# Optimization experiments

Measured on AMD Instinct MI355X. Metric: run time of the kernel, lower is better.

The kernel has to match this reference:

```python
import jax, jax.numpy as jnp
import numpy as np

B, T, D, NH = 16, 1024, 2048, 4
H_CYCLES, L_CYCLES = 2, 2


def _ln(x, g, b, eps=1e-5):
    m = jnp.mean(x, axis=-1, keepdims=True)
    v = jnp.mean((x - m) ** 2, axis=-1, keepdims=True)
    return (x - m) * jax.lax.rsqrt(v + eps) * g + b


def _mha(q_in, k_in, v_in, in_w, in_b, out_w, out_b):
    # torch nn.MultiheadAttention (batch_first) with packed in_proj
    d = q_in.shape[-1]
    hd = d // NH
    wq, wk, wv = jnp.split(in_w, 3, axis=0)
    bq, bk, bv = jnp.split(in_b, 3, axis=0)
    q = (q_in @ wq.T + bq).reshape(q_in.shape[0], -1, NH, hd)
    k = (k_in @ wk.T + bk).reshape(k_in.shape[0], -1, NH, hd)
    v = (v_in @ wv.T + bv).reshape(v_in.shape[0], -1, NH, hd)
    att = jnp.einsum('bqhd,bkhd->bhqk', q, k) / jnp.sqrt(jnp.asarray(hd, q.dtype))
    att = jax.nn.softmax(att, axis=-1)
    o = jnp.einsum('bhqk,bkhd->bqhd', att, v).reshape(q_in.shape[0], -1, d)
    return o @ out_w.T + out_b


def _block(z, inj, p):
    # CoTReasoningBlock
    x = z + inj
    n1 = _ln(x, p['n1_g'], p['n1_b'])
    x = x + _mha(n1, n1, n1, p['attn_in_w'], p['attn_in_b'], p['attn_out_w'], p['attn_out_b'])
    n2 = _ln(x, p['n2_g'], p['n2_b'])
    h = jax.nn.gelu(n2 @ p['f1_w'].T + p['f1_b'], approximate=False)
    return x + h @ p['f2_w'].T + p['f2_b']


def setup_inputs() -> dict:
    key = jax.random.key(0)
    ks = iter(jax.random.split(key, 32))

    def w(*shape):
        return jax.random.normal(next(ks), shape, jnp.float32) * 0.02

    inp = {}
    inp['x'] = jax.random.normal(next(ks), (B, T, D), jnp.float32)
    inp['global_query'] = w(1, 1, D)
    inp['attn_in_w'] = w(3 * D, D)
    inp['attn_in_b'] = jnp.zeros((3 * D,), jnp.float32)
    inp['attn_out_w'] = w(D, D)
    inp['attn_out_b'] = jnp.zeros((D,), jnp.float32)
    inp['mlp1_w'] = w(D, D)
    inp['mlp1_b'] = jnp.zeros((D,), jnp.float32)
    inp['mlp2_w'] = w(D, D)
    inp['mlp2_b'] = jnp.zeros((D,), jnp.float32)
    for pfx in ('h', 'l'):
        inp[pfx + '_attn_in_w'] = w(3 * D, D)
        inp[pfx + '_attn_in_b'] = jnp.zeros((3 * D,), jnp.float32)
        inp[pfx + '_attn_out_w'] = w(D, D)
        inp[pfx + '_attn_out_b'] = jnp.zeros((D,), jnp.float32)
        inp[pfx + '_n1_g'] = jnp.ones((D,), jnp.float32)
        inp[pfx + '_n1_b'] = jnp.zeros((D,), jnp.float32)
        inp[pfx + '_n2_g'] = jnp.ones((D,), jnp.float32)
        inp[pfx + '_n2_b'] = jnp.zeros((D,), jnp.float32)
        inp[pfx + '_f1_w'] = w(D, D)
        inp[pfx + '_f1_b'] = jnp.zeros((D,), jnp.float32)
        inp[pfx + '_f2_w'] = w(D, D)
        inp[pfx + '_f2_b'] = jnp.zeros((D,), jnp.float32)
    inp['norm_g'] = jnp.ones((D,), jnp.float32)
    inp['norm_b'] = jnp.zeros((D,), jnp.float32)
    return inp


def reference(x, global_query, attn_in_w, attn_in_b, attn_out_w, attn_out_b,
              mlp1_w, mlp1_b, mlp2_w, mlp2_b,
              h_attn_in_w, h_attn_in_b, h_attn_out_w, h_attn_out_b,
              h_n1_g, h_n1_b, h_n2_g, h_n2_b, h_f1_w, h_f1_b, h_f2_w, h_f2_b,
              l_attn_in_w, l_attn_in_b, l_attn_out_w, l_attn_out_b,
              l_n1_g, l_n1_b, l_n2_g, l_n2_b, l_f1_w, l_f1_b, l_f2_w, l_f2_b,
              norm_g, norm_b):
    Bd, Td, Dd = x.shape
    q = jnp.broadcast_to(global_query, (Bd, 1, Dd))
    a = _mha(q, x, x, attn_in_w, attn_in_b, attn_out_w, attn_out_b)  # (B,1,D)
    a = jax.nn.gelu(a @ mlp1_w.T + mlp1_b, approximate=False) @ mlp2_w.T + mlp2_b

    Hp = dict(attn_in_w=h_attn_in_w, attn_in_b=h_attn_in_b, attn_out_w=h_attn_out_w,
              attn_out_b=h_attn_out_b, n1_g=h_n1_g, n1_b=h_n1_b, n2_g=h_n2_g, n2_b=h_n2_b,
              f1_w=h_f1_w, f1_b=h_f1_b, f2_w=h_f2_w, f2_b=h_f2_b)
    Lp = dict(attn_in_w=l_attn_in_w, attn_in_b=l_attn_in_b, attn_out_w=l_attn_out_w,
              attn_out_b=l_attn_out_b, n1_g=l_n1_g, n1_b=l_n1_b, n2_g=l_n2_g, n2_b=l_n2_b,
              f1_w=l_f1_w, f1_b=l_f1_b, f2_w=l_f2_w, f2_b=l_f2_b)

    z0 = jnp.zeros((1, 1, Dd), x.dtype)

    def step(carry, xt):
        zH, zL = carry
        xt = xt[None]  # (1,1,D)
        zHn, zLn = zH, zL
        # torch.no_grad refinement phase. NOTE: the original code shadows the
        # loop variable `_`, so BOTH conditions test the inner L-cycle index;
        # with H_CYCLES==L_CYCLES==2 the last L cycle is skipped and the inner
        # zH update never fires. Reproduced exactly.
        for _h in range(H_CYCLES):
            for _l in range(L_CYCLES):
                if not (_l == H_CYCLES - 1 and _l == L_CYCLES - 1):
                    zLn = _block(zLn, zHn + xt, Lp)
            if L_CYCLES - 1 != H_CYCLES - 1:
                zHn = _block(zHn, zLn, Hp)
        zHg = jax.lax.stop_gradient(zHn)
        zLg = jax.lax.stop_gradient(zLn)
        # grad-enabled final updates
        zLg = _block(zLg, zHg + xt, Lp)
        zHg = _block(zHg, zLg, Hp)
        return (zHg, zLg), None

    (zH, zL), _ = jax.lax.scan(step, (z0, z0), a)
    return _ln(zH, norm_g, norm_b)  # (1,1,D)
```

## Files before the change

### kernel.cpp

```cpp
#include <hip/hip_runtime.h>
#include <hip/hip_bf16.h>

#define DD 2048
#define SCALE 0.04419417382415922f


__device__ __forceinline__ float waveReduceSum(float v) {
  #pragma unroll
  for (int off = 32; off; off >>= 1) v += __shfl_down(v, off);
  return v;
}

__device__ __forceinline__ float blockReduceSum(float v, float* sred) {
  v = waveReduceSum(v);
  int wid = threadIdx.x >> 6, lane = threadIdx.x & 63;
  if (lane == 0) sred[wid] = v;
  __syncthreads();
  float r = (sred[0] + sred[1]) + (sred[2] + sred[3]);
  __syncthreads();
  return r;
}

__device__ __forceinline__ float geluf(float x) {
  return 0.5f * x * (1.0f + erff(x * 0.7071067811865476f));
}


__global__ void k_zero(float* p, int n) {
  int i = blockIdx.x * 256 + threadIdx.x;
  if (i < n) p[i] = 0.0f;
}


template<int NADD, bool LN, bool GELU, bool RES>
__launch_bounds__(256)
__global__ void gemv1(const float* __restrict__ W, const float* __restrict__ bias,
                      const float* __restrict__ v0, const float* __restrict__ v1,
                      const float* __restrict__ v2,
                      const float* __restrict__ g, const float* __restrict__ bln,
                      float* __restrict__ y, float* __restrict__ xside)
{
  __shared__ __align__(16) float sx[DD];
  __shared__ float sred[4];
  int tid = threadIdx.x;
  float xv[8];
  #pragma unroll
  for (int i = 0; i < 8; ++i) {
    int idx = tid + i * 256;
    float v = v0[idx];
    if (NADD >= 1) v += v1[idx];
    if (NADD >= 2) v += v2[idx];
    xv[i] = v;
  }
  if (xside != nullptr && blockIdx.x == 0) {
    #pragma unroll
    for (int i = 0; i < 8; ++i) xside[tid + i * 256] = xv[i];
  }
  if (LN) {
    float s = 0.0f;
    #pragma unroll
    for (int i = 0; i < 8; ++i) s += xv[i];
    float mean = blockReduceSum(s, sred) * (1.0f / DD);
    float vs = 0.0f;
    #pragma unroll
    for (int i = 0; i < 8; ++i) { float d = xv[i] - mean; vs += d * d; }
    float var = blockReduceSum(vs, sred) * (1.0f / DD);
    float rs = 1.0f / sqrtf(var + 1e-5f);
    #pragma unroll
    for (int i = 0; i < 8; ++i) {
      int idx = tid + i * 256;
      sx[idx] = (xv[i] - mean) * rs * g[idx] + bln[idx];
    }
  } else {
    #pragma unroll
    for (int i = 0; i < 8; ++i) sx[tid + i * 256] = xv[i];
  }
  __syncthreads();

  int wid = tid >> 6, lane = tid & 63;
  int row = blockIdx.x * 4 + wid;
  const float4* Wr = (const float4*)(W + (size_t)row * DD);
  const float4* sx4 = (const float4*)sx;
  float acc = 0.0f;
  #pragma unroll
  for (int i = 0; i < 8; ++i) {
    float4 w4 = Wr[lane + i * 64];
    float4 x4 = sx4[lane + i * 64];
    acc += w4.x * x4.x + w4.y * x4.y + w4.z * x4.z + w4.w * x4.w;
  }
  acc = waveReduceSum(acc);
  if (lane == 0) {
    float val = acc + bias[row];
    if (GELU) val = geluf(val);
    if (RES) y[row] += val; else y[row] = val;
  }
}


__global__ void k_ufold(const float* __restrict__ Wfull, const float* __restrict__ qv,
                        float* __restrict__ u)
{
  int seg = blockIdx.x & 15, chunk = blockIdx.x >> 4;
  int h = seg >> 2;
  int tid = threadIdx.x;
  __shared__ float sq[128];
  if (tid < 128) sq[tid] = qv[seg * 128 + tid];
  __syncthreads();
  int d = chunk * 256 + tid;
  const float* Wp = Wfull + (size_t)(2048 + seg * 128) * DD + d;
  float acc = 0.0f;
  #pragma unroll 4
  for (int j = 0; j < 128; ++j) acc += Wp[(size_t)j * DD] * sq[j];
  atomicAdd(&u[(h << 11) + d], acc * SCALE);
}

__global__ void k_cfold(const float* __restrict__ qv, const float* __restrict__ inb,
                        float* __restrict__ c)
{
  __shared__ float sred[4];
  int tid = threadIdx.x;
  for (int h = 0; h < 4; ++h) {
    float s = 0.0f;
    for (int j = tid; j < 512; j += 256) s += qv[h * 512 + j] * inb[2048 + h * 512 + j];
    float tot = blockReduceSum(s, sred);
    if (tid == 0) c[h] = tot * SCALE;
    __syncthreads();
  }
}


__global__ void k_scores(const float* __restrict__ x, const float* __restrict__ u,
                         const float* __restrict__ c, float* __restrict__ sc)
{
  int blk = blockIdx.x;
  int b = blk >> 10, t = blk & 1023;
  int tid = threadIdx.x, wid = tid >> 6, lane = tid & 63;
  const float4* xr = (const float4*)(x + (size_t)blk * DD);
  float acc[4] = {0, 0, 0, 0};
  #pragma unroll
  for (int i = 0; i < 2; ++i) {
    int f = tid + i * 256;
    float4 x4 = xr[f];
    #pragma unroll
    for (int h = 0; h < 4; ++h) {
      float4 u4 = ((const float4*)(u + (h << 11)))[f];
      acc[h] += x4.x * u4.x + x4.y * u4.y + x4.z * u4.z + x4.w * u4.w;
    }
  }
  __shared__ float sred[4][4];
  #pragma unroll
  for (int h = 0; h < 4; ++h) {
    float v = waveReduceSum(acc[h]);
    if (lane == 0) sred[h][wid] = v;
  }
  __syncthreads();
  if (tid < 4) {
    float v = sred[tid][0] + sred[tid][1] + sred[tid][2] + sred[tid][3] + c[tid];
    sc[((size_t)(b * 4 + tid) << 10) + t] = v;
  }
}


__global__ void k_softmax(float* __restrict__ s)
{
  __shared__ float sred[4];
  int tid = threadIdx.x, wid = tid >> 6, lane = tid & 63;
  float* p = s + ((size_t)blockIdx.x << 10);
  float v[4];
  #pragma unroll
  for (int i = 0; i < 4; ++i) v[i] = p[tid + i * 256];
  float m = fmaxf(fmaxf(v[0], v[1]), fmaxf(v[2], v[3]));
  #pragma unroll
  for (int off = 32; off; off >>= 1) m = fmaxf(m, __shfl_down(m, off));
  if (lane == 0) sred[wid] = m;
  __syncthreads();
  m = fmaxf(fmaxf(sred[0], sred[1]), fmaxf(sred[2], sred[3]));
  __syncthreads();
  float e[4], sum = 0.0f;
  #pragma unroll
  for (int i = 0; i < 4; ++i) { e[i] = expf(v[i] - m); sum += e[i]; }
  float tot = blockReduceSum(sum, sred);
  float inv = 1.0f / tot;
  #pragma unroll
  for (int i = 0; i < 4; ++i) p[tid + i * 256] = e[i] * inv;
}


__global__ void k_xbar_part(const float* __restrict__ x, const float* __restrict__ att,
                            float* __restrict__ part)
{
  int blk = blockIdx.x;
  int seg = blk & 7, chunk = (blk >> 3) & 7, b = blk >> 6;
  int tid = threadIdx.x;
  __shared__ float satt[4][128];
  for (int i = tid; i < 512; i += 256) {
    int h = i >> 7, j = i & 127;
    satt[h][j] = att[((size_t)(b * 4 + h) << 10) + seg * 128 + j];
  }
  __syncthreads();
  int d = chunk * 256 + tid;
  const float* xb = x + ((size_t)b * 1024 + seg * 128) * DD + d;
  float a0 = 0, a1 = 0, a2 = 0, a3 = 0;
  #pragma unroll 4
  for (int j = 0; j < 128; ++j) {
    float xv = xb[(size_t)j * DD];
    a0 += satt[0][j] * xv; a1 += satt[1][j] * xv;
    a2 += satt[2][j] * xv; a3 += satt[3][j] * xv;
  }
  size_t base = ((size_t)(b * 8 + seg) * 4);
  part[((base + 0) << 11) + d] = a0;
  part[((base + 1) << 11) + d] = a1;
  part[((base + 2) << 11) + d] = a2;
  part[((base + 3) << 11) + d] = a3;
}

__global__ void k_xbar_red(const float* __restrict__ part, float* __restrict__ xbar)
{
  int i = blockIdx.x * 256 + threadIdx.x;
  int d = i & 2047; int h = (i >> 11) & 3; int b = i >> 13;
  float s = 0.0f;
  #pragma unroll
  for (int seg = 0; seg < 8; ++seg)
    s += part[(((size_t)(b * 8 + seg) * 4 + h) << 11) + d];
  xbar[i] = s;
}


__launch_bounds__(256)
__global__ void k_vproj(const float* __restrict__ inW, const float* __restrict__ inB,
                        const float* __restrict__ xbar, float* __restrict__ o)
{
  __shared__ __align__(16) float sv[8][DD];
  int tid = threadIdx.x, wid = tid >> 6, lane = tid & 63;
  int row0 = blockIdx.x * 8;
  int h = row0 >> 9;
  int rowA = row0 + wid, rowB = row0 + 4 + wid;
  const float4* WA = (const float4*)(inW + (size_t)(4096 + rowA) * DD);
  const float4* WB = (const float4*)(inW + (size_t)(4096 + rowB) * DD);
  float4 wa[8], wb[8];
  #pragma unroll
  for (int i = 0; i < 8; ++i) { wa[i] = WA[lane + i * 64]; wb[i] = WB[lane + i * 64]; }
  float accA[16], accB[16];
  #pragma unroll
  for (int b = 0; b < 16; ++b) { accA[b] = 0; accB[b] = 0; }
  for (int half = 0; half < 2; ++half) {
    __syncthreads();
    for (int i = tid; i < 8 * 512; i += 256) {
      int b = i >> 9, f = i & 511;
      ((float4*)&sv[b][0])[f] =
          ((const float4*)(xbar + (((size_t)(half * 8 + b) * 4 + h) << 11)))[f];
    }
    __syncthreads();
    #pragma unroll
    for (int i = 0; i < 8; ++i) {
      int f = lane + i * 64;
      #pragma unroll
      for (int b = 0; b < 8; ++b) {
        float4 x4 = ((const float4*)&sv[b][0])[f];
        accA[half * 8 + b] += wa[i].x * x4.x + wa[i].y * x4.y + wa[i].z * x4.z + wa[i].w * x4.w;
        accB[half * 8 + b] += wb[i].x * x4.x + wb[i].y * x4.y + wb[i].z * x4.z + wb[i].w * x4.w;
      }
    }
  }
  #pragma unroll
  for (int b = 0; b < 16; ++b) {
    float v = waveReduceSum(accA[b]);
    if (lane == 0) o[((size_t)b << 11) + rowA] = v + inB[4096 + rowA];
    v = waveReduceSum(accB[b]);
    if (lane == 0) o[((size_t)b << 11) + rowB] = v + inB[4096 + rowB];
  }
}


template<bool GELU>
__launch_bounds__(256)
__global__ void gemvB(const float* __restrict__ W, const float* __restrict__ bias,
                      const float* __restrict__ vin, float* __restrict__ y)
{
  __shared__ __align__(16) float sv[8][DD];
  int tid = threadIdx.x, wid = tid >> 6, lane = tid & 63;
  int row0 = blockIdx.x * 8;
  int rowA = row0 + wid, rowB = row0 + 4 + wid;
  const float4* WA = (const float4*)(W + (size_t)rowA * DD);
  const float4* WB = (const float4*)(W + (size_t)rowB * DD);
  float4 wa[8], wb[8];
  #pragma unroll
  for (int i = 0; i < 8; ++i) { wa[i] = WA[lane + i * 64]; wb[i] = WB[lane + i * 64]; }
  float accA[16], accB[16];
  #pragma unroll
  for (int b = 0; b < 16; ++b) { accA[b] = 0; accB[b] = 0; }
  for (int half = 0; half < 2; ++half) {
    __syncthreads();
    for (int i = tid; i < 8 * 512; i += 256) {
      int b = i >> 9, f = i & 511;
      ((float4*)&sv[b][0])[f] =
          ((const float4*)(vin + ((size_t)(half * 8 + b) << 11)))[f];
    }
    __syncthreads();
    #pragma unroll
    for (int i = 0; i < 8; ++i) {
      int f = lane + i * 64;
      #pragma unroll
      for (int b = 0; b < 8; ++b) {
        float4 x4 = ((const float4*)&sv[b][0])[f];
        accA[half * 8 + b] += wa[i].x * x4.x + wa[i].y * x4.y + wa[i].z * x4.z + wa[i].w * x4.w;
        accB[half * 8 + b] += wb[i].x * x4.x + wb[i].y * x4.y + wb[i].z * x4.z + wb[i].w * x4.w;
      }
    }
  }
  #pragma unroll
  for (int b = 0; b < 16; ++b) {
    float v = waveReduceSum(accA[b]);
    if (lane == 0) {
      float r = v + bias[rowA];
      if (GELU) r = geluf(r);
      y[((size_t)b << 11) + rowA] = r;
    }
    v = waveReduceSum(accB[b]);
    if (lane == 0) {
      float r = v + bias[rowB];
      if (GELU) r = geluf(r);
      y[((size_t)b << 11) + rowB] = r;
    }
  }
}


__global__ void k_final_ln(const float* __restrict__ z, const float* __restrict__ g,
                           const float* __restrict__ b, float* __restrict__ out)
{
  __shared__ float sred[4];
  int tid = threadIdx.x;
  float xv[8];
  #pragma unroll
  for (int i = 0; i < 8; ++i) xv[i] = z[tid + i * 256];
  float s = 0.0f;
  #pragma unroll
  for (int i = 0; i < 8; ++i) s += xv[i];
  float mean = blockReduceSum(s, sred) * (1.0f / DD);
  float vs = 0.0f;
  #pragma unroll
  for (int i = 0; i < 8; ++i) { float d = xv[i] - mean; vs += d * d; }
  float var = blockReduceSum(vs, sred) * (1.0f / DD);
  float rs = 1.0f / sqrtf(var + 1e-5f);
  #pragma unroll
  for (int i = 0; i < 8; ++i) {
    int idx = tid + i * 256;
    out[idx] = (xv[i] - mean) * rs * g[idx] + b[idx];
  }
}


struct BlockP {
  const float *in_w, *in_b, *out_w, *out_b, *n1g, *n1b, *n2g, *n2b, *f1w, *f1b, *f2w, *f2b;
};

static void runBlock(const BlockP& p, const float* z, float* xb,
                     const float* i1, const float* i2,
                     float* tbuf, float* hbuf, hipStream_t stream)
{
  const float* wv = p.in_w + (size_t)4096 * DD;
  const float* bv = p.in_b + 4096;
  if (i2)
    gemv1<2, true, false, false><<<512, 256, 0, stream>>>(wv, bv, z, i1, i2, p.n1g, p.n1b, tbuf, xb);
  else
    gemv1<1, true, false, false><<<512, 256, 0, stream>>>(wv, bv, z, i1, nullptr, p.n1g, p.n1b, tbuf, xb);
  gemv1<0, false, false, true><<<512, 256, 0, stream>>>(p.out_w, p.out_b, tbuf, nullptr, nullptr, nullptr, nullptr, xb, nullptr);
  gemv1<0, true, true, false><<<512, 256, 0, stream>>>(p.f1w, p.f1b, xb, nullptr, nullptr, p.n2g, p.n2b, hbuf, nullptr);
  gemv1<0, false, false, true><<<512, 256, 0, stream>>>(p.f2w, p.f2b, hbuf, nullptr, nullptr, nullptr, nullptr, xb, nullptr);
}

extern "C" void kernel_launch(void* const* d_in, const int* in_sizes, int n_in,
                              void* d_out, int out_size, void* d_ws, size_t ws_size,
                              hipStream_t stream)
{
  const float* x          = (const float*)d_in[0];
  const float* gq         = (const float*)d_in[1];
  const float* attn_in_w  = (const float*)d_in[2];
  const float* attn_in_b  = (const float*)d_in[3];
  const float* attn_out_w = (const float*)d_in[4];
  const float* attn_out_b = (const float*)d_in[5];
  const float* mlp1_w     = (const float*)d_in[6];
  const float* mlp1_b     = (const float*)d_in[7];
  const float* mlp2_w     = (const float*)d_in[8];
  const float* mlp2_b     = (const float*)d_in[9];
  BlockP Hp = { (const float*)d_in[10], (const float*)d_in[11], (const float*)d_in[12],
                (const float*)d_in[13], (const float*)d_in[14], (const float*)d_in[15],
                (const float*)d_in[16], (const float*)d_in[17], (const float*)d_in[18],
                (const float*)d_in[19], (const float*)d_in[20], (const float*)d_in[21] };
  BlockP Lp = { (const float*)d_in[22], (const float*)d_in[23], (const float*)d_in[24],
                (const float*)d_in[25], (const float*)d_in[26], (const float*)d_in[27],
                (const float*)d_in[28], (const float*)d_in[29], (const float*)d_in[30],
                (const float*)d_in[31], (const float*)d_in[32], (const float*)d_in[33] };
  const float* norm_g = (const float*)d_in[34];
  const float* norm_b = (const float*)d_in[35];

  float* ws = (float*)d_ws;
  float* u     = ws + 0;
  float* zL[2] = { ws + 8192,  ws + 12288 };
  float* zH[2] = { ws + 10240, ws + 14336 };
  float* qv    = ws + 16384;
  float* c     = ws + 18432;
  float* tbuf  = ws + 18496;
  float* hbuf  = ws + 20544;
  float* sc    = ws + 22592;
  float* xbar  = ws + 88128;
  float* o     = ws + 219200;
  float* a0    = ws + 251968;
  float* a1    = ws + 284736;
  float* abuf  = ws + 317504;
  float* part  = ws + 350272;

  k_zero<<<48, 256, 0, stream>>>(ws, 12288);

  gemv1<0, false, false, false><<<512, 256, 0, stream>>>(
      attn_in_w, attn_in_b, gq, nullptr, nullptr, nullptr, nullptr, qv, nullptr);
  k_ufold<<<128, 256, 0, stream>>>(attn_in_w, qv, u);
  k_cfold<<<1, 256, 0, stream>>>(qv, attn_in_b, c);
  k_scores<<<16384, 256, 0, stream>>>(x, u, c, sc);
  k_softmax<<<64, 256, 0, stream>>>(sc);
  k_xbar_part<<<1024, 256, 0, stream>>>(x, sc, part);
  k_xbar_red<<<512, 256, 0, stream>>>(part, xbar);
  k_vproj<<<256, 256, 0, stream>>>(attn_in_w, attn_in_b, xbar, o);
  gemvB<false><<<256, 256, 0, stream>>>(attn_out_w, attn_out_b, o, a0);
  gemvB<true ><<<256, 256, 0, stream>>>(mlp1_w, mlp1_b, a0, a1);
  gemvB<false><<<256, 256, 0, stream>>>(mlp2_w, mlp2_b, a1, abuf);

  int li = 0, hi = 0;
  for (int s = 0; s < 16; ++s) {
    const float* xt = abuf + (size_t)s * DD;
    for (int r = 0; r < 3; ++r) {
      runBlock(Lp, zL[li], zL[li ^ 1], zH[hi], xt, tbuf, hbuf, stream);
      li ^= 1;
    }
    runBlock(Hp, zH[hi], zH[hi ^ 1], zL[li], nullptr, tbuf, hbuf, stream);
    hi ^= 1;
  }

  k_final_ln<<<1, 256, 0, stream>>>(zH[hi], norm_g, norm_b, (float*)d_out);
}
```

Measured before the change: 1.996 ms.

## Fuse recurrent scan into one persistent kernel with hierarchical grid barriers

Replaces the roughly 256 small per-stage GEMV launches of the sequential scan with a single persistent kernel of 512 blocks that runs every stage in turn. Stages are separated by a two-level atomic grid barrier (8 groups of 64 blocks feeding a root counter), and the final LayerNorm is folded into the same kernel. This is meant to remove kernel launch and drain overhead on the serial critical path. LayerNorm statistics now come from a single fused sum and sum-of-squares reduction, and loads are vectorised. The risks are barrier latency, deadlock if all 512 blocks cannot be co-resident, and a small numerical change from the one-pass variance.

```diff
diff --git a/kernel.cpp b/kernel.cpp
--- a/kernel.cpp
+++ b/kernel.cpp
@@ -18,6 +18,18 @@
   __syncthreads();
   float r = (sred[0] + sred[1]) + (sred[2] + sred[3]);
   __syncthreads();
+  return r;
+}
+
+__device__ __forceinline__ float2 blockReduce2(float s, float ss, float* sred) {
+  #pragma unroll
+  for (int off = 32; off; off >>= 1) { s += __shfl_down(s, off); ss += __shfl_down(ss, off); }
+  int wid = threadIdx.x >> 6, lane = threadIdx.x & 63;
+  if (lane == 0) { sred[wid] = s; sred[4 + wid] = ss; }
+  __syncthreads();
+  float2 r;
+  r.x = (sred[0] + sred[1]) + (sred[2] + sred[3]);
+  r.y = (sred[4] + sred[5]) + (sred[6] + sred[7]);
   return r;
 }
 
@@ -41,7 +53,7 @@
                       float* __restrict__ y, float* __restrict__ xside)
 {
   __shared__ __align__(16) float sx[DD];
-  __shared__ float sred[4];
+  __shared__ float sred[8];
   int tid = threadIdx.x;
   float xv[8];
   #pragma unroll
@@ -117,7 +129,7 @@
 __global__ void k_cfold(const float* __restrict__ qv, const float* __restrict__ inb,
                         float* __restrict__ c)
 {
-  __shared__ float sred[4];
+  __shared__ float sred[8];
   int tid = threadIdx.x;
   for (int h = 0; h < 4; ++h) {
     float s = 0.0f;
@@ -128,7 +140,6 @@
   }
 }
 
-
 __global__ void k_scores(const float* __restrict__ x, const float* __restrict__ u,
                          const float* __restrict__ c, float* __restrict__ sc)
 {
@@ -160,10 +171,9 @@
   }
 }
 
-
 __global__ void k_softmax(float* __restrict__ s)
 {
-  __shared__ float sred[4];
+  __shared__ float sred[8];
   int tid = threadIdx.x, wid = tid >> 6, lane = tid & 63;
   float* p = s + ((size_t)blockIdx.x << 10);
   float v[4];
@@ -184,7 +194,6 @@
   #pragma unroll
   for (int i = 0; i < 4; ++i) p[tid + i * 256] = e[i] * inv;
 }
-
 
 __global__ void k_xbar_part(const float* __restrict__ x, const float* __restrict__ att,
                             float* __restrict__ part)
@@ -225,7 +234,6 @@
   xbar[i] = s;
 }
 
-
 __launch_bounds__(256)
 __global__ void k_vproj(const float* __restrict__ inW, const float* __restrict__ inB,
                         const float* __restrict__ xbar, float* __restrict__ o)
@@ -271,7 +279,6 @@
   }
 }
 
-
 template<bool GELU>
 __launch_bounds__(256)
 __global__ void gemvB(const float* __restrict__ W, const float* __restrict__ bias,
@@ -326,49 +333,165 @@
 }
 
 
-__global__ void k_final_ln(const float* __restrict__ z, const float* __restrict__ g,
-                           const float* __restrict__ b, float* __restrict__ out)
-{
-  __shared__ float sred[4];
-  int tid = threadIdx.x;
-  float xv[8];
-  #pragma unroll
-  for (int i = 0; i < 8; ++i) xv[i] = z[tid + i * 256];
-  float s = 0.0f;
-  #pragma unroll
-  for (int i = 0; i < 8; ++i) s += xv[i];
-  float mean = blockReduceSum(s, sred) * (1.0f / DD);
-  float vs = 0.0f;
-  #pragma unroll
-  for (int i = 0; i < 8; ++i) { float d = xv[i] - mean; vs += d * d; }
-  float var = blockReduceSum(vs, sred) * (1.0f / DD);
-  float rs = 1.0f / sqrtf(var + 1e-5f);
+struct ScanArgs {
+  const float *Lwv, *Lbv, *Low, *Lob, *Lf1, *Lf1b, *Lf2, *Lf2b;
+  const float *Ln1g, *Ln1b, *Ln2g, *Ln2b;
+  const float *Hwv, *Hbv, *How, *Hob, *Hf1, *Hf1b, *Hf2, *Hf2b;
+  const float *Hn1g, *Hn1b, *Hn2g, *Hn2b;
+  const float *abuf;
+  float *zL0, *zL1, *zH0, *zH1, *tbuf, *hbuf;
+  const float *norm_g, *norm_b;
+  float *out;
+  unsigned *root, *grp;
+};
+
+__device__ __forceinline__ void gridBar(unsigned* root, unsigned* grp, int epoch) {
+  __syncthreads();
+  if (threadIdx.x == 0) {
+    unsigned g = (unsigned)blockIdx.x >> 6;
+    unsigned old = __hip_atomic_fetch_add(&grp[g * 32], 1u,
+                                          __ATOMIC_ACQ_REL, __HIP_MEMORY_SCOPE_AGENT);
+    if (old == 64u * (unsigned)epoch - 1u)
+      __hip_atomic_fetch_add(root, 1u, __ATOMIC_RELEASE, __HIP_MEMORY_SCOPE_AGENT);
+    unsigned target = 8u * (unsigned)epoch;
+    while (__hip_atomic_load(root, __ATOMIC_RELAXED, __HIP_MEMORY_SCOPE_AGENT) < target) {
+      __builtin_amdgcn_s_sleep(1);
+    }
+    __builtin_amdgcn_fence(__ATOMIC_ACQUIRE, "agent");
+  }
+  __syncthreads();
+}
+
+template<int NADD, bool LN, bool GELU, bool RES, bool XSIDE>
+__device__ __forceinline__ void stage(
+    const float* __restrict__ W, const float* __restrict__ bias,
+    const float* __restrict__ v0, const float* __restrict__ v1,
+    const float* __restrict__ v2,
+    const float* __restrict__ g, const float* __restrict__ bln,
+    float* __restrict__ y, float* __restrict__ xside,
+    float* sx, float* sred)
+{
+  int tid = threadIdx.x, wid = tid >> 6, lane = tid & 63;
+  int row = blockIdx.x * 4 + wid;
+  const float4* Wr = (const float4*)(W + (size_t)row * DD);
+  float4 wa[8];
+  #pragma unroll
+  for (int i = 0; i < 8; ++i) wa[i] = Wr[lane + i * 64];
+
+  float4 xv[2];
+  #pragma unroll
+  for (int i = 0; i < 2; ++i) {
+    int idx = tid + i * 256;
+    float4 a = ((const float4*)v0)[idx];
+    if (NADD >= 1) { float4 b = ((const float4*)v1)[idx];
+                     a.x += b.x; a.y += b.y; a.z += b.z; a.w += b.w; }
+    if (NADD >= 2) { float4 b = ((const float4*)v2)[idx];
+                     a.x += b.x; a.y += b.y; a.z += b.z; a.w += b.w; }
+    xv[i] = a;
+  }
+  if (XSIDE && blockIdx.x == 0) {
+    #pragma unroll
+    for (int i = 0; i < 2; ++i) ((float4*)xside)[tid + i * 256] = xv[i];
+  }
+  if (LN) {
+    float s = 0.0f, ss = 0.0f;
+    #pragma unroll
+    for (int i = 0; i < 2; ++i) {
+      s  += xv[i].x + xv[i].y + xv[i].z + xv[i].w;
+      ss += xv[i].x * xv[i].x + xv[i].y * xv[i].y + xv[i].z * xv[i].z + xv[i].w * xv[i].w;
+    }
+    float2 r = blockReduce2(s, ss, sred);
+    float mean = r.x * (1.0f / DD);
+    float var = r.y * (1.0f / DD) - mean * mean;
+    float rs = 1.0f / sqrtf(var + 1e-5f);
+    #pragma unroll
+    for (int i = 0; i < 2; ++i) {
+      int idx = tid + i * 256;
+      float4 g4 = ((const float4*)g)[idx];
+      float4 b4 = ((const float4*)bln)[idx];
+      float4 t;
+      t.x = (xv[i].x - mean) * rs * g4.x + b4.x;
+      t.y = (xv[i].y - mean) * rs * g4.y + b4.y;
+      t.z = (xv[i].z - mean) * rs * g4.z + b4.z;
+      t.w = (xv[i].w - mean) * rs * g4.w + b4.w;
+      ((float4*)sx)[idx] = t;
+    }
+  } else {
+    #pragma unroll
+    for (int i = 0; i < 2; ++i) ((float4*)sx)[tid + i * 256] = xv[i];
+  }
+  __syncthreads();
+  const float4* sx4 = (const float4*)sx;
+  float acc = 0.0f;
   #pragma unroll
   for (int i = 0; i < 8; ++i) {
-    int idx = tid + i * 256;
-    out[idx] = (xv[i] - mean) * rs * g[idx] + b[idx];
-  }
-}
-
-
-struct BlockP {
-  const float *in_w, *in_b, *out_w, *out_b, *n1g, *n1b, *n2g, *n2b, *f1w, *f1b, *f2w, *f2b;
-};
-
-static void runBlock(const BlockP& p, const float* z, float* xb,
-                     const float* i1, const float* i2,
-                     float* tbuf, float* hbuf, hipStream_t stream)
-{
-  const float* wv = p.in_w + (size_t)4096 * DD;
-  const float* bv = p.in_b + 4096;
-  if (i2)
-    gemv1<2, true, false, false><<<512, 256, 0, stream>>>(wv, bv, z, i1, i2, p.n1g, p.n1b, tbuf, xb);
-  else
-    gemv1<1, true, false, false><<<512, 256, 0, stream>>>(wv, bv, z, i1, nullptr, p.n1g, p.n1b, tbuf, xb);
-  gemv1<0, false, false, true><<<512, 256, 0, stream>>>(p.out_w, p.out_b, tbuf, nullptr, nullptr, nullptr, nullptr, xb, nullptr);
-  gemv1<0, true, true, false><<<512, 256, 0, stream>>>(p.f1w, p.f1b, xb, nullptr, nullptr, p.n2g, p.n2b, hbuf, nullptr);
-  gemv1<0, false, false, true><<<512, 256, 0, stream>>>(p.f2w, p.f2b, hbuf, nullptr, nullptr, nullptr, nullptr, xb, nullptr);
-}
+    float4 x4 = sx4[lane + i * 64];
+    acc += wa[i].x * x4.x + wa[i].y * x4.y + wa[i].z * x4.z + wa[i].w * x4.w;
+  }
+  acc = waveReduceSum(acc);
+  if (lane == 0) {
+    float val = acc + bias[row];
+    if (GELU) val = geluf(val);
+    if (RES) y[row] += val; else y[row] = val;
+  }
+}
+
+__global__ __launch_bounds__(256, 2) void k_scan(ScanArgs a)
+{
+  __shared__ __align__(16) float sx[DD];
+  __shared__ float sred[8];
+  float* zL[2] = { a.zL0, a.zL1 };
+  float* zH[2] = { a.zH0, a.zH1 };
+  int li = 0, hi = 0;
+  int epoch = 0;
+  #define BAR() gridBar(a.root, a.grp, ++epoch)
+
+  for (int s = 0; s < 16; ++s) {
+    const float* xt = a.abuf + (size_t)s * DD;
+    for (int r = 0; r < 3; ++r) {
+      stage<2, true, false, false, true >(a.Lwv, a.Lbv, zL[li], zH[hi], xt,
+                                          a.Ln1g, a.Ln1b, a.tbuf, zL[li ^ 1], sx, sred); BAR();
+      stage<0, false, false, true, false>(a.Low, a.Lob, a.tbuf, nullptr, nullptr,
+                                          nullptr, nullptr, zL[li ^ 1], nullptr, sx, sred); BAR();
+      stage<0, true, true, false, false>(a.Lf1, a.Lf1b, zL[li ^ 1], nullptr, nullptr,
+                                          a.Ln2g, a.Ln2b, a.hbuf, nullptr, sx, sred); BAR();
+      stage<0, false, false, true, false>(a.Lf2, a.Lf2b, a.hbuf, nullptr, nullptr,
+                                          nullptr, nullptr, zL[li ^ 1], nullptr, sx, sred); BAR();
+      li ^= 1;
+    }
+    stage<1, true, false, false, true >(a.Hwv, a.Hbv, zH[hi], zL[li], nullptr,
+                                        a.Hn1g, a.Hn1b, a.tbuf, zH[hi ^ 1], sx, sred); BAR();
+    stage<0, false, false, true, false>(a.How, a.Hob, a.tbuf, nullptr, nullptr,
+                                        nullptr, nullptr, zH[hi ^ 1], nullptr, sx, sred); BAR();
+    stage<0, true, true, false, false>(a.Hf1, a.Hf1b, zH[hi ^ 1], nullptr, nullptr,
+                                        a.Hn2g, a.Hn2b, a.hbuf, nullptr, sx, sred); BAR();
+    stage<0, false, false, true, false>(a.Hf2, a.Hf2b, a.hbuf, nullptr, nullptr,
+                                        nullptr, nullptr, zH[hi ^ 1], nullptr, sx, sred); BAR();
+    hi ^= 1;
+  }
+  #undef BAR
+
+  if (blockIdx.x == 0) {
+    int tid = threadIdx.x;
+    const float* z = zH[hi];
+    float xv[8];
+    #pragma unroll
+    for (int i = 0; i < 8; ++i) xv[i] = z[tid + i * 256];
+    float s = 0.0f, ss = 0.0f;
+    #pragma unroll
+    for (int i = 0; i < 8; ++i) { s += xv[i]; ss += xv[i] * xv[i]; }
+    float2 r = blockReduce2(s, ss, sred);
+    float mean = r.x * (1.0f / DD);
+    float var = r.y * (1.0f / DD) - mean * mean;
+    float rs = 1.0f / sqrtf(var + 1e-5f);
+    #pragma unroll
+    for (int i = 0; i < 8; ++i) {
+      int idx = tid + i * 256;
+      a.out[idx] = (xv[i] - mean) * rs * a.norm_g[idx] + a.norm_b[idx];
+    }
+  }
+}
+
 
 extern "C" void kernel_launch(void* const* d_in, const int* in_sizes, int n_in,
                               void* d_out, int out_size, void* d_ws, size_t ws_size,
@@ -384,34 +507,28 @@
   const float* mlp1_b     = (const float*)d_in[7];
   const float* mlp2_w     = (const float*)d_in[8];
   const float* mlp2_b     = (const float*)d_in[9];
-  BlockP Hp = { (const float*)d_in[10], (const float*)d_in[11], (const float*)d_in[12],
-                (const float*)d_in[13], (const float*)d_in[14], (const float*)d_in[15],
-                (const float*)d_in[16], (const float*)d_in[17], (const float*)d_in[18],
-                (const float*)d_in[19], (const float*)d_in[20], (const float*)d_in[21] };
-  BlockP Lp = { (const float*)d_in[22], (const float*)d_in[23], (const float*)d_in[24],
-                (const float*)d_in[25], (const float*)d_in[26], (const float*)d_in[27],
-                (const float*)d_in[28], (const float*)d_in[29], (const float*)d_in[30],
-                (const float*)d_in[31], (const float*)d_in[32], (const float*)d_in[33] };
-  const float* norm_g = (const float*)d_in[34];
-  const float* norm_b = (const float*)d_in[35];
 
   float* ws = (float*)d_ws;
-  float* u     = ws + 0;
-  float* zL[2] = { ws + 8192,  ws + 12288 };
-  float* zH[2] = { ws + 10240, ws + 14336 };
-  float* qv    = ws + 16384;
-  float* c     = ws + 18432;
-  float* tbuf  = ws + 18496;
-  float* hbuf  = ws + 20544;
-  float* sc    = ws + 22592;
-  float* xbar  = ws + 88128;
-  float* o     = ws + 219200;
-  float* a0    = ws + 251968;
-  float* a1    = ws + 284736;
-  float* abuf  = ws + 317504;
-  float* part  = ws + 350272;
-
-  k_zero<<<48, 256, 0, stream>>>(ws, 12288);
+  unsigned* root = (unsigned*)ws;
+  unsigned* grp  = (unsigned*)(ws + 16);
+  float* u     = ws + 512;
+  float* zL0   = ws + 8704;
+  float* zL1   = ws + 10752;
+  float* zH0   = ws + 12800;
+  float* zH1   = ws + 14848;
+  float* tbuf  = ws + 16896;
+  float* hbuf  = ws + 18944;
+  float* qv    = ws + 20992;
+  float* c     = ws + 23040;
+  float* sc    = ws + 23104;
+  float* xbar  = ws + 88640;
+  float* o     = ws + 219712;
+  float* a0    = ws + 252480;
+  float* a1    = ws + 285248;
+  float* abuf  = ws + 318016;
+  float* part  = ws + 350784;
+
+  k_zero<<<66, 256, 0, stream>>>(ws, 16896);
 
   gemv1<0, false, false, false><<<512, 256, 0, stream>>>(
       attn_in_w, attn_in_b, gq, nullptr, nullptr, nullptr, nullptr, qv, nullptr);
@@ -426,16 +543,30 @@
   gemvB<true ><<<256, 256, 0, stream>>>(mlp1_w, mlp1_b, a0, a1);
   gemvB<false><<<256, 256, 0, stream>>>(mlp2_w, mlp2_b, a1, abuf);
 
-  int li = 0, hi = 0;
-  for (int s = 0; s < 16; ++s) {
-    const float* xt = abuf + (size_t)s * DD;
-    for (int r = 0; r < 3; ++r) {
-      runBlock(Lp, zL[li], zL[li ^ 1], zH[hi], xt, tbuf, hbuf, stream);
-      li ^= 1;
-    }
-    runBlock(Hp, zH[hi], zH[hi ^ 1], zL[li], nullptr, tbuf, hbuf, stream);
-    hi ^= 1;
-  }
-
-  k_final_ln<<<1, 256, 0, stream>>>(zH[hi], norm_g, norm_b, (float*)d_out);
-}
+  ScanArgs sa;
+  sa.Hwv = (const float*)d_in[10] + (size_t)4096 * DD;
+  sa.Hbv = (const float*)d_in[11] + 4096;
+  sa.How = (const float*)d_in[12];
+  sa.Hob = (const float*)d_in[13];
+  sa.Hn1g = (const float*)d_in[14]; sa.Hn1b = (const float*)d_in[15];
+  sa.Hn2g = (const float*)d_in[16]; sa.Hn2b = (const float*)d_in[17];
+  sa.Hf1 = (const float*)d_in[18]; sa.Hf1b = (const float*)d_in[19];
+  sa.Hf2 = (const float*)d_in[20]; sa.Hf2b = (const float*)d_in[21];
+  sa.Lwv = (const float*)d_in[22] + (size_t)4096 * DD;
+  sa.Lbv = (const float*)d_in[23] + 4096;
+  sa.Low = (const float*)d_in[24];
+  sa.Lob = (const float*)d_in[25];
+  sa.Ln1g = (const float*)d_in[26]; sa.Ln1b = (const float*)d_in[27];
+  sa.Ln2g = (const float*)d_in[28]; sa.Ln2b = (const float*)d_in[29];
+  sa.Lf1 = (const float*)d_in[30]; sa.Lf1b = (const float*)d_in[31];
+  sa.Lf2 = (const float*)d_in[32]; sa.Lf2b = (const float*)d_in[33];
+  sa.abuf = abuf;
+  sa.zL0 = zL0; sa.zL1 = zL1; sa.zH0 = zH0; sa.zH1 = zH1;
+  sa.tbuf = tbuf; sa.hbuf = hbuf;
+  sa.norm_g = (const float*)d_in[34];
+  sa.norm_b = (const float*)d_in[35];
+  sa.out = (float*)d_out;
+  sa.root = root; sa.grp = grp;
+
+  k_scan<<<512, 256, 0, stream>>>(sa);
+}
```

New measurement: 5.314 ms. 2.66x slower.
